# Kernel optimization log

Hardware: AMD Instinct MI355X
Metric: run time of the kernel (lower is better)

## Reference

```python
import jax, jax.numpy as jnp
import numpy as np

N = 50000      # n_nodes == ninput
E = 800000     # edges
NHID = 96
N_INTER = 6
EPS = 1e-12


def _l2norm(x):
    # F.normalize(x, p=2, dim=1) with eps=1e-12
    n = jnp.linalg.norm(x, axis=1, keepdims=True)
    return x / jnp.maximum(n, EPS)


def _sage(x, src, dst, Wl, bl, Wr, n):
    # PyG SAGEConv (mean aggr): lin_l(mean_{j in N(i)} x_j) + lin_r(x_i)
    agg = jax.ops.segment_sum(x[src], dst, num_segments=n)          # [N, nhid]
    deg = jax.ops.segment_sum(jnp.ones((src.shape[0],), x.dtype), dst, num_segments=n)
    agg = agg / jnp.maximum(deg, 1.0)[:, None]
    return agg @ Wl + bl + x @ Wr


def _mlp(x, W1, b1, W2, b2, W3, b3):
    # GNN-Bet score MLP (eval mode, dropout p=0): nhid -> 2*nhid -> 2*nhid -> 1
    h = jax.nn.relu(x @ W1 + b1)
    h = jax.nn.relu(h @ W2 + b2)
    return h @ W3 + b3


def setup_inputs() -> dict:
    key = jax.random.key(0)
    ks = jax.random.split(key, 16)
    s = 0.05
    inp = {
        'edge_index1': jax.random.randint(ks[0], (2, E), 0, N, dtype=jnp.int32),
        'edge_vals1': jax.random.uniform(ks[1], (E,), dtype=jnp.float32),
        'edge_index2': jax.random.randint(ks[2], (2, E), 0, N, dtype=jnp.int32),
        # GNN_Layer_Init: weight [ninput=N, nhid], bias [nhid]
        'gc1_W': jax.random.normal(ks[3], (N, NHID), dtype=jnp.float32) * s,
        'gc1_b': jnp.zeros((NHID,), jnp.float32),
        # 7 SAGEConv layers (6 intermediate + gc_last), stacked
        'sage_Wl': jax.random.normal(ks[4], (7, NHID, NHID), dtype=jnp.float32) * s,
        'sage_bl': jnp.zeros((7, NHID), jnp.float32),
        'sage_Wr': jax.random.normal(ks[5], (7, NHID, NHID), dtype=jnp.float32) * s,
        # score MLP
        'mlp_W1': jax.random.normal(ks[6], (NHID, 2 * NHID), dtype=jnp.float32) * s,
        'mlp_b1': jnp.zeros((2 * NHID,), jnp.float32),
        'mlp_W2': jax.random.normal(ks[7], (2 * NHID, 2 * NHID), dtype=jnp.float32) * s,
        'mlp_b2': jnp.zeros((2 * NHID,), jnp.float32),
        'mlp_W3': jax.random.normal(ks[8], (2 * NHID, 1), dtype=jnp.float32) * s,
        'mlp_b3': jnp.zeros((1,), jnp.float32),
    }
    return inp


def reference(edge_index1, edge_vals1, edge_index2, gc1_W, gc1_b,
              sage_Wl, sage_bl, sage_Wr,
              mlp_W1, mlp_b1, mlp_W2, mlp_b2, mlp_W3, mlp_b3):
    # gc1: spmm(adj1, W) -> out[i] = sum_j adj1[i,j] * W[j]
    dst1, src1 = edge_index1[0], edge_index1[1]
    h0 = jax.ops.segment_sum(gc1_W[src1] * edge_vals1[:, None], dst1, num_segments=N) + gc1_b
    x2_1 = _l2norm(jax.nn.relu(h0))

    src2, dst2 = edge_index2[0], edge_index2[1]

    # main trunk: 6 intermediate SAGE layers applied sequentially
    x = x2_1
    for i in range(N_INTER):
        x = _l2norm(jax.nn.relu(_sage(x, src2, dst2, sage_Wl[i], sage_bl[i], sage_Wr[i], N)))
    x_last = jax.nn.relu(_sage(x, src2, dst2, sage_Wl[N_INTER], sage_bl[N_INTER], sage_Wr[N_INTER], N))

    # scores: MLP on x2_1, on each intermediate layer applied once to x2_1, and on x_last
    score = _mlp(x2_1, mlp_W1, mlp_b1, mlp_W2, mlp_b2, mlp_W3, mlp_b3)
    for i in range(N_INTER):
        xi = _l2norm(jax.nn.relu(_sage(x2_1, src2, dst2, sage_Wl[i], sage_bl[i], sage_Wr[i], N)))
        score = score + _mlp(xi, mlp_W1, mlp_b1, mlp_W2, mlp_b2, mlp_W3, mlp_b3)
    score = score + _mlp(x_last, mlp_W1, mlp_b1, mlp_W2, mlp_b2, mlp_W3, mlp_b3)
    return score  # [N, 1]
```

## Files before the change

kernel.cpp:

```cpp
#include <hip/hip_runtime.h>

#define NH 96
#define NH2 192

typedef __attribute__((ext_vector_type(8))) short short8;
typedef __attribute__((ext_vector_type(4))) float f32x4;

__device__ __forceinline__ unsigned short f2b(float f) {
  unsigned u = __float_as_uint(f);
  unsigned r = (u + 0x7FFFu + ((u >> 16) & 1u)) >> 16;
  return (unsigned short)r;
}
__device__ __forceinline__ float blo(unsigned w) { return __uint_as_float(w << 16); }
__device__ __forceinline__ float bhi(unsigned w) { return __uint_as_float(w & 0xFFFF0000u); }
__device__ __forceinline__ float b2f(short v) { return __uint_as_float(((unsigned)(unsigned short)v) << 16); }

__device__ __forceinline__ unsigned cvt_pk(float lo, float hi) {
  unsigned r;
  asm("v_cvt_pk_bf16_f32 %0, %1, %2" : "=v"(r) : "v"(lo), "v"(hi));
  return r;
}

__device__ __forceinline__ short8 u4_to_s8(int a, int b, int c, int d) {
  union { int u[4]; short8 s; } x;
  x.u[0] = a; x.u[1] = b; x.u[2] = c; x.u[3] = d;
  return x.s;
}

#define MFMA(a, b, c) __builtin_amdgcn_mfma_f32_16x16x32_bf16((a), (b), (c), 0, 0, 0)
#define WFRAG(p, idx) (*(const short8*)((p) + ((idx) << 9) + (l << 3)))

__device__ __forceinline__ void stage(unsigned short* dst, const unsigned short* src, int nshorts,
                                      int tid, int nt) {
  const uint4* s = (const uint4*)src;
  uint4* d = (uint4*)dst;
  int nv = nshorts >> 3;
  for (int i = tid; i < nv; i += nt) d[i] = s[i];
}

__device__ __forceinline__ short8 xchg(unsigned p0lo, unsigned p0hi, unsigned p1lo, unsigned p1hi,
                                       int srcA, int srcB, int hi) {
  int a0 = __shfl((int)p0lo, srcA), a1 = __shfl((int)p0hi, srcA);
  int c0 = __shfl((int)p1lo, srcA), c1 = __shfl((int)p1hi, srcA);
  int b0 = __shfl((int)p0lo, srcB), b1 = __shfl((int)p0hi, srcB);
  int d0 = __shfl((int)p1lo, srcB), d1 = __shfl((int)p1hi, srcB);
  return u4_to_s8(hi ? c0 : a0, hi ? c1 : a1, hi ? d0 : b0, hi ? d1 : b1);
}

__device__ __forceinline__ void gather_mean(const int* __restrict__ rp, const int* __restrict__ csrc,
                                            const unsigned short* __restrict__ X,
                                            int nd, int g, short8 af[3]) {
  int s = rp[nd], e = rp[nd + 1];
  float aa[3][8], bb[3][8];
#pragma unroll
  for (int kf = 0; kf < 3; ++kf)
#pragma unroll
    for (int j = 0; j < 8; ++j) { aa[kf][j] = 0.f; bb[kf][j] = 0.f; }

  const unsigned short* Xg = X + g * 8;
  int i = s;
  for (; i + 3 < e; i += 4) {
    const unsigned short* x0 = Xg + (size_t)csrc[i] * NH;
    const unsigned short* x1 = Xg + (size_t)csrc[i + 1] * NH;
    const unsigned short* x2 = Xg + (size_t)csrc[i + 2] * NH;
    const unsigned short* x3 = Xg + (size_t)csrc[i + 3] * NH;
    short8 r00 = *(const short8*)(x0), r01 = *(const short8*)(x0 + 32), r02 = *(const short8*)(x0 + 64);
    short8 r10 = *(const short8*)(x1), r11 = *(const short8*)(x1 + 32), r12 = *(const short8*)(x1 + 64);
    short8 r20 = *(const short8*)(x2), r21 = *(const short8*)(x2 + 32), r22 = *(const short8*)(x2 + 64);
    short8 r30 = *(const short8*)(x3), r31 = *(const short8*)(x3 + 32), r32 = *(const short8*)(x3 + 64);
#pragma unroll
    for (int j = 0; j < 8; ++j) {
      aa[0][j] += b2f(r00[j]) + b2f(r20[j]);
      aa[1][j] += b2f(r01[j]) + b2f(r21[j]);
      aa[2][j] += b2f(r02[j]) + b2f(r22[j]);
      bb[0][j] += b2f(r10[j]) + b2f(r30[j]);
      bb[1][j] += b2f(r11[j]) + b2f(r31[j]);
      bb[2][j] += b2f(r12[j]) + b2f(r32[j]);
    }
  }
  for (; i < e; ++i) {
    const unsigned short* x0 = Xg + (size_t)csrc[i] * NH;
    short8 r0 = *(const short8*)(x0), r1 = *(const short8*)(x0 + 32), r2 = *(const short8*)(x0 + 64);
#pragma unroll
    for (int j = 0; j < 8; ++j) {
      aa[0][j] += b2f(r0[j]); aa[1][j] += b2f(r1[j]); aa[2][j] += b2f(r2[j]);
    }
  }
  float inv = 1.f / fmaxf((float)(e - s), 1.f);
#pragma unroll
  for (int kf = 0; kf < 3; ++kf)
#pragma unroll
    for (int j = 0; j < 8; ++j) af[kf][j] = (short)f2b((aa[kf][j] + bb[kf][j]) * inv);
}


__global__ void k_count(const int* __restrict__ dst1, const int* __restrict__ dst2,
                        int* __restrict__ cnt1, int* __restrict__ cnt2, int E, int psize, int cblocks,
                        const float* __restrict__ Wl, const float* __restrict__ Wr,
                        const float* __restrict__ W1, const float* __restrict__ W2,
                        const float* __restrict__ gW,
                        unsigned short* __restrict__ Wlp, unsigned short* __restrict__ Wrp,
                        unsigned short* __restrict__ W1p, unsigned short* __restrict__ W2p,
                        unsigned short* __restrict__ gwb, int gtotal) {
  if (blockIdx.x < (unsigned)cblocks) {
    int p = blockIdx.x & 7;
    int e = (blockIdx.x >> 3) * blockDim.x + threadIdx.x;
    if (e >= E) return;
    int lo = p * psize, hi = lo + psize;
    int d = dst1[e];
    if (d >= lo && d < hi) atomicAdd(&cnt1[d], 1);
    int dd = dst2[e];
    if (dd >= lo && dd < hi) atomicAdd(&cnt2[dd], 1);
    return;
  }
  int t = (blockIdx.x - cblocks) * blockDim.x + threadIdx.x;
  if (t < 129024) {
    bool isR = t >= 64512;
    int u = isR ? t - 64512 : t;
    int i = u / 9216, v = u % 9216;
    int tt = v / 1536, r = v % 1536;
    int kf = r / 512, w = r % 512, l = w >> 3, j = w & 7;
    int c = l & 15, g = l >> 4;
    int k = kf * 32 + g * 8 + j, nn = tt * 16 + c;
    float val = (isR ? Wr : Wl)[i * 9216 + k * 96 + nn];
    (isR ? Wrp : Wlp)[u] = f2b(val);
  } else if (t < 147456) {
    int u = t - 129024;
    int tt = u / 1536, r = u % 1536;
    int kf = r / 512, w = r % 512, l = w >> 3, j = w & 7;
    int c = l & 15, g = l >> 4;
    int k = kf * 32 + g * 8 + j, nn = tt * 16 + c;
    W1p[u] = f2b(W1[k * 192 + nn]);
  } else if (t < 184320) {
    int u = t - 147456;
    int tt = u / 3072, r = u % 3072;
    int kf = r / 512, w = r % 512, l = w >> 3, j = w & 7;
    int c = l & 15, g = l >> 4;
    int k = kf * 32 + g * 8 + j, nn = tt * 16 + c;
    W2p[u] = f2b(W2[k * 192 + nn]);
  } else {
    int i = (t - 184320) * 4;
    if (i + 3 < gtotal) {
      float4 v = *(const float4*)(gW + i);
      ushort4 o;
      o.x = f2b(v.x); o.y = f2b(v.y); o.z = f2b(v.z); o.w = f2b(v.w);
      *(ushort4*)(gwb + i) = o;
    }
  }
}


__global__ __launch_bounds__(256) void k_scanA(const int* __restrict__ cnt1, const int* __restrict__ cnt2,
                                               int* __restrict__ bs, int n) {
  int seg = blockIdx.y;
  const int* cnt = seg ? cnt2 : cnt1;
  int t = threadIdx.x;
  int idx = blockIdx.x * 1024 + t * 4;
  int sum = 0;
  if (idx + 3 < n) {
    int4 v = *(const int4*)(cnt + idx);
    sum = v.x + v.y + v.z + v.w;
  } else {
    for (int j = 0; j < 4; ++j) if (idx + j < n) sum += cnt[idx + j];
  }
  __shared__ int s[256];
  s[t] = sum;
  __syncthreads();
  for (int off = 128; off > 0; off >>= 1) {
    if (t < off) s[t] += s[t + off];
    __syncthreads();
  }
  if (t == 0) bs[seg * 64 + blockIdx.x] = s[0];
}

__global__ __launch_bounds__(128) void k_scanB(int* __restrict__ bs, int* __restrict__ rp1,
                                               int* __restrict__ rp2, int nb, int n) {
  int w = threadIdx.x >> 6, l = threadIdx.x & 63;
  int v = (l < nb) ? bs[w * 64 + l] : 0;
  int incl = v;
  for (int off = 1; off < 64; off <<= 1) {
    int u = __shfl_up(incl, off);
    if (l >= off) incl += u;
  }
  if (l < nb) bs[w * 64 + l] = incl - v;
  if (l == 63) {
    int* rp = w ? rp2 : rp1;
    rp[n] = incl;
  }
}

__global__ __launch_bounds__(256) void k_scanC(const int* __restrict__ cnt1, const int* __restrict__ cnt2,
                                               const int* __restrict__ bs,
                                               int* __restrict__ rp1, int* __restrict__ cur1,
                                               int* __restrict__ rp2, int* __restrict__ cur2, int n) {
  int seg = blockIdx.y;
  const int* cnt = seg ? cnt2 : cnt1;
  int* rp = seg ? rp2 : rp1;
  int* cur = seg ? cur2 : cur1;
  int t = threadIdx.x;
  int idx = blockIdx.x * 1024 + t * 4;
  int v[4] = {0, 0, 0, 0};
  if (idx + 3 < n) {
    int4 q = *(const int4*)(cnt + idx);
    v[0] = q.x; v[1] = q.y; v[2] = q.z; v[3] = q.w;
  } else {
    for (int j = 0; j < 4; ++j) if (idx + j < n) v[j] = cnt[idx + j];
  }
  int tsum = v[0] + v[1] + v[2] + v[3];
  __shared__ int s[256];
  s[t] = tsum;
  __syncthreads();
  for (int off = 1; off < 256; off <<= 1) {
    int u = (t >= off) ? s[t - off] : 0;
    __syncthreads();
    s[t] += u;
    __syncthreads();
  }
  int run = (t == 0 ? 0 : s[t - 1]) + bs[seg * 64 + blockIdx.x];
  for (int j = 0; j < 4; ++j) {
    if (idx + j < n) {
      rp[idx + j] = run;
      cur[idx + j] = run;
      run += v[j];
    }
  }
}

__global__ __launch_bounds__(1024) void k_scan(const int* __restrict__ cnt, int* __restrict__ rp,
                                               int* __restrict__ cur, int n) {
  __shared__ int s[1024];
  int tid = threadIdx.x;
  int chunk = (n + 1023) >> 10;
  int beg = tid * chunk;
  int end = min(beg + chunk, n);
  int sum = 0;
  for (int i = beg; i < end; ++i) sum += cnt[i];
  s[tid] = sum;
  __syncthreads();
  for (int off = 1; off < 1024; off <<= 1) {
    int v = (tid >= off) ? s[tid - off] : 0;
    __syncthreads();
    s[tid] += v;
    __syncthreads();
  }
  int excl = (tid == 0) ? 0 : s[tid - 1];
  for (int i = beg; i < end; ++i) { rp[i] = excl; cur[i] = excl; excl += cnt[i]; }
  if (tid == 1023) rp[n] = s[1023];
}

__global__ void k_scatter(const int* __restrict__ d1, const int* __restrict__ s1, const float* __restrict__ v1,
                          int* __restrict__ cur1, int2* __restrict__ c1sv,
                          const int* __restrict__ s2, const int* __restrict__ d2,
                          int* __restrict__ cur2, int* __restrict__ c2s, int E, int psize) {
  int p = blockIdx.x & 7;
  int e = (blockIdx.x >> 3) * blockDim.x + threadIdx.x;
  if (e >= E) return;
  int lo = p * psize, hi = lo + psize;
  int d = d1[e];
  if (d >= lo && d < hi) {
    int pos = atomicAdd(&cur1[d], 1);
    c1sv[pos] = make_int2(s1[e], __float_as_int(v1[e]));
  }
  int dd = d2[e];
  if (dd >= lo && dd < hi) {
    int pos = atomicAdd(&cur2[dd], 1);
    c2s[pos] = s2[e];
  }
}


__global__ __launch_bounds__(256) void k_gc1(const int* __restrict__ rp, const int2* __restrict__ cv,
                                             const unsigned short* __restrict__ Wb,
                                             const float* __restrict__ b, unsigned short* __restrict__ out, int n) {
  int gw = (blockIdx.x * 256 + threadIdx.x) >> 6;
  int l = threadIdx.x & 63;
  if (gw >= n) return;
  int s = rp[gw], e = rp[gw + 1];
  bool act = l < 48;
  float a0 = 0.f, a1 = 0.f, b0 = 0.f, b1 = 0.f, c0 = 0.f, c1 = 0.f, d0 = 0.f, d1 = 0.f;
  int i = s;
  for (; i + 3 < e; i += 4) {
    int2 q0 = cv[i], q1 = cv[i + 1], q2 = cv[i + 2], q3 = cv[i + 3];
    if (act) {
      unsigned w0 = *(const unsigned*)(Wb + (size_t)q0.x * NH + 2 * l);
      unsigned w1 = *(const unsigned*)(Wb + (size_t)q1.x * NH + 2 * l);
      unsigned w2 = *(const unsigned*)(Wb + (size_t)q2.x * NH + 2 * l);
      unsigned w3 = *(const unsigned*)(Wb + (size_t)q3.x * NH + 2 * l);
      float v0 = __int_as_float(q0.y), v1 = __int_as_float(q1.y);
      float v2 = __int_as_float(q2.y), v3 = __int_as_float(q3.y);
      a0 = fmaf(v0, blo(w0), a0); a1 = fmaf(v0, bhi(w0), a1);
      b0 = fmaf(v1, blo(w1), b0); b1 = fmaf(v1, bhi(w1), b1);
      c0 = fmaf(v2, blo(w2), c0); c1 = fmaf(v2, bhi(w2), c1);
      d0 = fmaf(v3, blo(w3), d0); d1 = fmaf(v3, bhi(w3), d1);
    }
  }
  for (; i < e; ++i) {
    int2 q0 = cv[i];
    if (act) {
      unsigned w0 = *(const unsigned*)(Wb + (size_t)q0.x * NH + 2 * l);
      float v0 = __int_as_float(q0.y);
      a0 = fmaf(v0, blo(w0), a0); a1 = fmaf(v0, bhi(w0), a1);
    }
  }
  a0 += b0 + c0 + d0; a1 += b1 + c1 + d1;
  if (act) {
    a0 = fmaxf(a0 + b[2 * l], 0.f);
    a1 = fmaxf(a1 + b[2 * l + 1], 0.f);
  } else { a0 = a1 = 0.f; }
  float ss = a0 * a0 + a1 * a1;
#pragma unroll
  for (int o = 1; o < 64; o <<= 1) ss += __shfl_xor(ss, o);
  float sc = 1.f / fmaxf(sqrtf(ss), 1e-12f);
  if (act) {
    unsigned pk = ((unsigned)f2b(a1 * sc) << 16) | f2b(a0 * sc);
    ((unsigned*)out)[(size_t)gw * 48 + l] = pk;
  }
}


__global__ __launch_bounds__(256) void k_agg(const int* __restrict__ rp, const int* __restrict__ csrc,
                                             const unsigned short* __restrict__ X,
                                             unsigned short* __restrict__ out, int n) {
  int gw = (blockIdx.x * 256 + threadIdx.x) >> 6;
  int l = threadIdx.x & 63;
  if (gw >= n) return;
  int s = rp[gw], e = rp[gw + 1];
  bool act = l < 48;
  float a0 = 0.f, a1 = 0.f, b0 = 0.f, b1 = 0.f, c0 = 0.f, c1 = 0.f, d0 = 0.f, d1 = 0.f;
  int i = s;
  for (; i + 3 < e; i += 4) {
    int s0 = csrc[i], s1 = csrc[i + 1], s2 = csrc[i + 2], s3 = csrc[i + 3];
    if (act) {
      unsigned w0 = *(const unsigned*)(X + (size_t)s0 * NH + 2 * l);
      unsigned w1 = *(const unsigned*)(X + (size_t)s1 * NH + 2 * l);
      unsigned w2 = *(const unsigned*)(X + (size_t)s2 * NH + 2 * l);
      unsigned w3 = *(const unsigned*)(X + (size_t)s3 * NH + 2 * l);
      a0 += blo(w0); a1 += bhi(w0);
      b0 += blo(w1); b1 += bhi(w1);
      c0 += blo(w2); c1 += bhi(w2);
      d0 += blo(w3); d1 += bhi(w3);
    }
  }
  for (; i < e; ++i) {
    int s0 = csrc[i];
    if (act) {
      unsigned w0 = *(const unsigned*)(X + (size_t)s0 * NH + 2 * l);
      a0 += blo(w0); a1 += bhi(w0);
    }
  }
  a0 += b0 + c0 + d0; a1 += b1 + c1 + d1;
  float inv = 1.f / fmaxf((float)(e - s), 1.f);
  if (act) {
    unsigned pk = ((unsigned)f2b(a1 * inv) << 16) | f2b(a0 * inv);
    ((unsigned*)out)[(size_t)gw * 48 + l] = pk;
  }
}


template <int EPI>
__device__ __forceinline__ void sage_body(int blk, int nwaves, unsigned short* sw,
                                          const int* __restrict__ rp, const int* __restrict__ csrc,
                                          const unsigned short* __restrict__ X,
                                          const unsigned short* __restrict__ Wlp,
                                          const unsigned short* __restrict__ Wrp,
                                          const float* __restrict__ bias,
                                          unsigned short* __restrict__ Y, int n) {
  int tid = threadIdx.x;
  int l = tid & 63;
  int m0 = (blk * nwaves + (tid >> 6)) * 16;
  int c = l & 15, g = l >> 4;

  stage(sw, Wlp, 9216, tid, nwaves * 64);
  stage(sw + 9216, Wrp, 9216, tid, nwaves * 64);
  __syncthreads();

  int nd = min(m0 + c, n - 1);
  short8 af[3];
  gather_mean(rp, csrc, X, nd, g, af);

  size_t aoff = (size_t)nd * NH + g * 8;
  short8 xf[3];
#pragma unroll
  for (int kf = 0; kf < 3; ++kf) xf[kf] = *(const short8*)(X + aoff + kf * 32);

  f32x4 acc[6];
#pragma unroll
  for (int t = 0; t < 6; ++t) acc[t] = (f32x4){0.f, 0.f, 0.f, 0.f};
#pragma unroll
  for (int kf = 0; kf < 3; ++kf) {
#pragma unroll
    for (int t = 0; t < 6; ++t) {
      short8 wlf = WFRAG(sw, t * 3 + kf);
      acc[t] = MFMA(wlf, af[kf], acc[t]);
    }
#pragma unroll
    for (int t = 0; t < 6; ++t) {
      short8 wrf = WFRAG(sw + 9216, t * 3 + kf);
      acc[t] = MFMA(wrf, xf[kf], acc[t]);
    }
  }

  float v[6][4];
  float ss = 0.f;
#pragma unroll
  for (int t = 0; t < 6; ++t) {
    float4 bv = *(const float4*)(bias + t * 16 + g * 4);
#pragma unroll
    for (int r = 0; r < 4; ++r) {
      float x = fmaxf(acc[t][r] + ((const float*)&bv)[r], 0.f);
      v[t][r] = x;
      ss = fmaf(x, x, ss);
    }
  }
  if (EPI == 0) {
    ss += __shfl_xor(ss, 16);
    ss += __shfl_xor(ss, 32);
    float sc = 1.f / fmaxf(sqrtf(ss), 1e-12f);
#pragma unroll
    for (int t = 0; t < 6; ++t)
#pragma unroll
      for (int r = 0; r < 4; ++r) v[t][r] *= sc;
  }
  if (m0 + c < n) {
    unsigned short* yr = Y + (size_t)(m0 + c) * NH;
#pragma unroll
    for (int t = 0; t < 6; ++t)
      *(uint2*)(yr + t * 16 + g * 4) = make_uint2(cvt_pk(v[t][0], v[t][1]), cvt_pk(v[t][2], v[t][3]));
  }
}

template <int EPI>
__global__ __launch_bounds__(256) void k_sageagg(const int* __restrict__ rp, const int* __restrict__ csrc,
                                                 const unsigned short* __restrict__ X,
                                                 const unsigned short* __restrict__ Wlp,
                                                 const unsigned short* __restrict__ Wrp,
                                                 const float* __restrict__ bias,
                                                 unsigned short* __restrict__ Y, int n) {
  __shared__ __align__(16) unsigned short sw[18432];
  sage_body<EPI>(blockIdx.x, 4, sw, rp, csrc, X, Wlp, Wrp, bias, Y, n);
}


__global__ __launch_bounds__(512) void k_last(const int* __restrict__ rp, const int* __restrict__ csrc,
                                              const unsigned short* __restrict__ X,
                                              const unsigned short* __restrict__ Wlp,
                                              const unsigned short* __restrict__ Wrp,
                                              const float* __restrict__ bias,
                                              const unsigned short* __restrict__ W1p, const float* __restrict__ b1,
                                              const unsigned short* __restrict__ W2p, const float* __restrict__ b2,
                                              const float* __restrict__ W3, const float* __restrict__ b3,
                                              float* __restrict__ score, int n) {
  __shared__ __align__(16) unsigned short sw[18432];
  int tid = threadIdx.x;
  int l = tid & 63;
  int m0 = (blockIdx.x * 8 + (tid >> 6)) * 16;
  int c = l & 15, g = l >> 4;
  int srcA = c + ((g & 1) << 5), srcB = srcA + 16, hi = g >> 1;

  stage(sw, Wlp, 9216, tid, 512);
  stage(sw + 9216, Wrp, 9216, tid, 512);
  __syncthreads();

  int nd = min(m0 + c, n - 1);
  short8 af[3];
  gather_mean(rp, csrc, X, nd, g, af);

  size_t aoff = (size_t)nd * NH + g * 8;
  short8 xf[3];
#pragma unroll
  for (int kf = 0; kf < 3; ++kf) xf[kf] = *(const short8*)(X + aoff + kf * 32);

  f32x4 acc[6];
#pragma unroll
  for (int t = 0; t < 6; ++t) acc[t] = (f32x4){0.f, 0.f, 0.f, 0.f};
#pragma unroll
  for (int kf = 0; kf < 3; ++kf) {
#pragma unroll
    for (int t = 0; t < 6; ++t) {
      short8 wlf = WFRAG(sw, t * 3 + kf);
      acc[t] = MFMA(wlf, af[kf], acc[t]);
    }
#pragma unroll
    for (int t = 0; t < 6; ++t) {
      short8 wrf = WFRAG(sw + 9216, t * 3 + kf);
      acc[t] = MFMA(wrf, xf[kf], acc[t]);
    }
  }

  unsigned pk[6][2];
#pragma unroll
  for (int t = 0; t < 6; ++t) {
    float4 bv = *(const float4*)(bias + t * 16 + g * 4);
    float x0 = fmaxf(acc[t][0] + bv.x, 0.f);
    float x1 = fmaxf(acc[t][1] + bv.y, 0.f);
    float x2 = fmaxf(acc[t][2] + bv.z, 0.f);
    float x3 = fmaxf(acc[t][3] + bv.w, 0.f);
    pk[t][0] = cvt_pk(x0, x1);
    pk[t][1] = cvt_pk(x2, x3);
  }

  __syncthreads();
  stage(sw, W1p, 18432, tid, 512);
  short8 af1[3];
#pragma unroll
  for (int kf = 0; kf < 3; ++kf)
    af1[kf] = xchg(pk[2 * kf][0], pk[2 * kf][1], pk[2 * kf + 1][0], pk[2 * kf + 1][1], srcA, srcB, hi);
  __syncthreads();

  unsigned pk1[12][2];
#pragma unroll
  for (int t = 0; t < 12; ++t) {
    f32x4 a0 = (f32x4){0.f, 0.f, 0.f, 0.f};
#pragma unroll
    for (int kf = 0; kf < 3; ++kf) {
      short8 wf = WFRAG(sw, t * 3 + kf);
      a0 = MFMA(wf, af1[kf], a0);
    }
    float4 bv = *(const float4*)(b1 + t * 16 + g * 4);
    pk1[t][0] = cvt_pk(fmaxf(a0[0] + bv.x, 0.f), fmaxf(a0[1] + bv.y, 0.f));
    pk1[t][1] = cvt_pk(fmaxf(a0[2] + bv.z, 0.f), fmaxf(a0[3] + bv.w, 0.f));
  }

  short8 af2[6];
#pragma unroll
  for (int kf = 0; kf < 6; ++kf)
    af2[kf] = xchg(pk1[2 * kf][0], pk1[2 * kf][1], pk1[2 * kf + 1][0], pk1[2 * kf + 1][1], srcA, srcB, hi);

  float sv = 0.f;
#pragma unroll
  for (int h = 0; h < 2; ++h) {
    __syncthreads();
    stage(sw, W2p + h * 18432, 18432, tid, 512);
    __syncthreads();
#pragma unroll
    for (int tt = 0; tt < 6; ++tt) {
      int t = h * 6 + tt;
      f32x4 a0 = (f32x4){0.f, 0.f, 0.f, 0.f};
#pragma unroll
      for (int kf = 0; kf < 6; ++kf) {
        short8 wf = WFRAG(sw, tt * 6 + kf);
        a0 = MFMA(wf, af2[kf], a0);
      }
      float4 bv = *(const float4*)(b2 + t * 16 + g * 4);
      float4 wv3 = *(const float4*)(W3 + t * 16 + g * 4);
#pragma unroll
      for (int r = 0; r < 4; ++r)
        sv = fmaf(fmaxf(a0[r] + ((const float*)&bv)[r], 0.f), ((const float*)&wv3)[r], sv);
    }
  }
  sv += __shfl_xor(sv, 16);
  sv += __shfl_xor(sv, 32);
  if (g == 0 && m0 + c < n) score[m0 + c] += sv + b3[0];
}


__device__ __forceinline__ void branch_body(int bb, int blk, unsigned short* sw,
                                            const unsigned short* __restrict__ Ag,
                                            const unsigned short* __restrict__ X21,
                                            const unsigned short* __restrict__ Wlp,
                                            const unsigned short* __restrict__ Wrp,
                                            const float* __restrict__ sbl,
                                            const unsigned short* __restrict__ W1p, const float* __restrict__ b1,
                                            const unsigned short* __restrict__ W2p, const float* __restrict__ b2,
                                            const float* __restrict__ W3, const float* __restrict__ b3,
                                            unsigned short* __restrict__ Xb, float* __restrict__ score, int n) {
  int tid = threadIdx.x;
  int l = tid & 63;
  int m0 = (blk * 8 + (tid >> 6)) * 32;
  int c = l & 15, g = l >> 4;
  int srcA = c + ((g & 1) << 5), srcB = srcA + 16, hi = g >> 1;
  int rA = min(m0 + c, n - 1), rB = min(m0 + 16 + c, n - 1);
  size_t aoffA = (size_t)rA * NH + g * 8, aoffB = (size_t)rB * NH + g * 8;

  short8 af1[2][3];

  if (bb < 6) {
    const float* bl = sbl + (size_t)bb * NH;
    stage(sw, Wlp + (size_t)bb * 9216, 9216, tid, 512);
    stage(sw + 9216, Wrp + (size_t)bb * 9216, 9216, tid, 512);

    short8 agf[2][3], xf[2][3];
#pragma unroll
    for (int kf = 0; kf < 3; ++kf) {
      agf[0][kf] = *(const short8*)(Ag + aoffA + kf * 32);
      agf[1][kf] = *(const short8*)(Ag + aoffB + kf * 32);
      xf[0][kf] = *(const short8*)(X21 + aoffA + kf * 32);
      xf[1][kf] = *(const short8*)(X21 + aoffB + kf * 32);
    }
    __syncthreads();

    float v[2][6][4];
    float ss0 = 0.f, ss1 = 0.f;
#pragma unroll
    for (int t = 0; t < 6; ++t) {
      f32x4 a0 = (f32x4){0.f, 0.f, 0.f, 0.f};
      f32x4 a1 = (f32x4){0.f, 0.f, 0.f, 0.f};
#pragma unroll
      for (int kf = 0; kf < 3; ++kf) {
        short8 wlf = WFRAG(sw, t * 3 + kf);
        a0 = MFMA(wlf, agf[0][kf], a0);
        a1 = MFMA(wlf, agf[1][kf], a1);
        short8 wrf = WFRAG(sw + 9216, t * 3 + kf);
        a0 = MFMA(wrf, xf[0][kf], a0);
        a1 = MFMA(wrf, xf[1][kf], a1);
      }
      float4 bv = *(const float4*)(bl + t * 16 + g * 4);
#pragma unroll
      for (int r = 0; r < 4; ++r) {
        float x0 = fmaxf(a0[r] + ((const float*)&bv)[r], 0.f);
        float x1 = fmaxf(a1[r] + ((const float*)&bv)[r], 0.f);
        v[0][t][r] = x0; ss0 = fmaf(x0, x0, ss0);
        v[1][t][r] = x1; ss1 = fmaf(x1, x1, ss1);
      }
    }
    ss0 += __shfl_xor(ss0, 16); ss0 += __shfl_xor(ss0, 32);
    ss1 += __shfl_xor(ss1, 16); ss1 += __shfl_xor(ss1, 32);
    float sc0 = 1.f / fmaxf(sqrtf(ss0), 1e-12f);
    float sc1 = 1.f / fmaxf(sqrtf(ss1), 1e-12f);

    unsigned pk[2][6][2];
#pragma unroll
    for (int t = 0; t < 6; ++t) {
      pk[0][t][0] = cvt_pk(v[0][t][0] * sc0, v[0][t][1] * sc0);
      pk[0][t][1] = cvt_pk(v[0][t][2] * sc0, v[0][t][3] * sc0);
      pk[1][t][0] = cvt_pk(v[1][t][0] * sc1, v[1][t][1] * sc1);
      pk[1][t][1] = cvt_pk(v[1][t][2] * sc1, v[1][t][3] * sc1);
    }
    if (bb == 0) {
      if (m0 + c < n) {
        unsigned short* yr = Xb + (size_t)(m0 + c) * NH;
#pragma unroll
        for (int t = 0; t < 6; ++t) *(uint2*)(yr + t * 16 + g * 4) = make_uint2(pk[0][t][0], pk[0][t][1]);
      }
      if (m0 + 16 + c < n) {
        unsigned short* yr = Xb + (size_t)(m0 + 16 + c) * NH;
#pragma unroll
        for (int t = 0; t < 6; ++t) *(uint2*)(yr + t * 16 + g * 4) = make_uint2(pk[1][t][0], pk[1][t][1]);
      }
    }

    __syncthreads();
    stage(sw, W1p, 18432, tid, 512);
#pragma unroll
    for (int kf = 0; kf < 3; ++kf) {
      af1[0][kf] = xchg(pk[0][2 * kf][0], pk[0][2 * kf][1], pk[0][2 * kf + 1][0], pk[0][2 * kf + 1][1], srcA, srcB, hi);
      af1[1][kf] = xchg(pk[1][2 * kf][0], pk[1][2 * kf][1], pk[1][2 * kf + 1][0], pk[1][2 * kf + 1][1], srcA, srcB, hi);
    }
    __syncthreads();
  } else {
#pragma unroll
    for (int kf = 0; kf < 3; ++kf) {
      af1[0][kf] = *(const short8*)(X21 + aoffA + kf * 32);
      af1[1][kf] = *(const short8*)(X21 + aoffB + kf * 32);
    }
    stage(sw, W1p, 18432, tid, 512);
    __syncthreads();
  }

  unsigned pk1[2][12][2];
#pragma unroll
  for (int t = 0; t < 12; ++t) {
    f32x4 a0 = (f32x4){0.f, 0.f, 0.f, 0.f};
    f32x4 a1 = (f32x4){0.f, 0.f, 0.f, 0.f};
#pragma unroll
    for (int kf = 0; kf < 3; ++kf) {
      short8 wf = WFRAG(sw, t * 3 + kf);
      a0 = MFMA(wf, af1[0][kf], a0);
      a1 = MFMA(wf, af1[1][kf], a1);
    }
    float4 bv = *(const float4*)(b1 + t * 16 + g * 4);
    pk1[0][t][0] = cvt_pk(fmaxf(a0[0] + bv.x, 0.f), fmaxf(a0[1] + bv.y, 0.f));
    pk1[0][t][1] = cvt_pk(fmaxf(a0[2] + bv.z, 0.f), fmaxf(a0[3] + bv.w, 0.f));
    pk1[1][t][0] = cvt_pk(fmaxf(a1[0] + bv.x, 0.f), fmaxf(a1[1] + bv.y, 0.f));
    pk1[1][t][1] = cvt_pk(fmaxf(a1[2] + bv.z, 0.f), fmaxf(a1[3] + bv.w, 0.f));
  }

  short8 af2[2][6];
#pragma unroll
  for (int kf = 0; kf < 6; ++kf) {
    af2[0][kf] = xchg(pk1[0][2 * kf][0], pk1[0][2 * kf][1], pk1[0][2 * kf + 1][0], pk1[0][2 * kf + 1][1], srcA, srcB, hi);
    af2[1][kf] = xchg(pk1[1][2 * kf][0], pk1[1][2 * kf][1], pk1[1][2 * kf + 1][0], pk1[1][2 * kf + 1][1], srcA, srcB, hi);
  }
  float sv0 = 0.f, sv1 = 0.f;
#pragma unroll
  for (int h = 0; h < 2; ++h) {
    __syncthreads();
    stage(sw, W2p + h * 18432, 18432, tid, 512);
    __syncthreads();
#pragma unroll
    for (int tt = 0; tt < 6; ++tt) {
      int t = h * 6 + tt;
      f32x4 a0 = (f32x4){0.f, 0.f, 0.f, 0.f};
      f32x4 a1 = (f32x4){0.f, 0.f, 0.f, 0.f};
#pragma unroll
      for (int kf = 0; kf < 6; ++kf) {
        short8 wf = WFRAG(sw, tt * 6 + kf);
        a0 = MFMA(wf, af2[0][kf], a0);
        a1 = MFMA(wf, af2[1][kf], a1);
      }
      float4 bv = *(const float4*)(b2 + t * 16 + g * 4);
      float4 wv3 = *(const float4*)(W3 + t * 16 + g * 4);
#pragma unroll
      for (int r = 0; r < 4; ++r) {
        sv0 = fmaf(fmaxf(a0[r] + ((const float*)&bv)[r], 0.f), ((const float*)&wv3)[r], sv0);
        sv1 = fmaf(fmaxf(a1[r] + ((const float*)&bv)[r], 0.f), ((const float*)&wv3)[r], sv1);
      }
    }
  }
  sv0 += __shfl_xor(sv0, 16); sv0 += __shfl_xor(sv0, 32);
  sv1 += __shfl_xor(sv1, 16); sv1 += __shfl_xor(sv1, 32);
  if (g == 0) {
    float b3v = b3[0];
    if (m0 + c < n) atomicAdd(&score[m0 + c], sv0 + b3v);
    if (m0 + 16 + c < n) atomicAdd(&score[m0 + 16 + c], sv1 + b3v);
  }
}

__global__ __launch_bounds__(512) void k_branchA(const unsigned short* __restrict__ Ag,
                                                 const unsigned short* __restrict__ X21,
                                                 const unsigned short* __restrict__ Wlp,
                                                 const unsigned short* __restrict__ Wrp,
                                                 const float* __restrict__ sbl,
                                                 const unsigned short* __restrict__ W1p, const float* __restrict__ b1,
                                                 const unsigned short* __restrict__ W2p, const float* __restrict__ b2,
                                                 const float* __restrict__ W3, const float* __restrict__ b3,
                                                 unsigned short* __restrict__ Xb, float* __restrict__ score,
                                                 int n, int nblk) {
  __shared__ __align__(16) unsigned short sw[18432];
  int bb = (blockIdx.x >= (unsigned)nblk) ? 6 : 0;
  int blk = blockIdx.x - (bb ? nblk : 0);
  branch_body(bb, blk, sw, Ag, X21, Wlp, Wrp, sbl, W1p, b1, W2p, b2, W3, b3, Xb, score, n);
}

__global__ __launch_bounds__(512) void k_mega(const unsigned short* __restrict__ Ag,
                                              const unsigned short* __restrict__ X21,
                                              const unsigned short* __restrict__ Wlp,
                                              const unsigned short* __restrict__ Wrp,
                                              const float* __restrict__ sbl,
                                              const unsigned short* __restrict__ W1p, const float* __restrict__ b1,
                                              const unsigned short* __restrict__ W2p, const float* __restrict__ b2,
                                              const float* __restrict__ W3, const float* __restrict__ b3,
                                              float* __restrict__ score,
                                              const int* __restrict__ rp2, const int* __restrict__ c2s,
                                              const unsigned short* __restrict__ Xb, unsigned short* __restrict__ Tb,
                                              int n, int nblk, int nbranch) {
  __shared__ __align__(16) unsigned short sw[18432];
  if (blockIdx.x < (unsigned)nbranch) {
    int bb = 1 + blockIdx.x / nblk;
    int blk = blockIdx.x - (bb - 1) * nblk;
    branch_body(bb, blk, sw, Ag, X21, Wlp, Wrp, sbl, W1p, b1, W2p, b2, W3, b3, nullptr, score, n);
  } else {
    sage_body<0>(blockIdx.x - nbranch, 8, sw, rp2, c2s, Xb,
                 Wlp + 9216, Wrp + 9216, sbl + NH, Tb, n);
  }
}


extern "C" void kernel_launch(void* const* d_in, const int* in_sizes, int n_in,
                              void* d_out, int out_size, void* d_ws, size_t ws_size,
                              hipStream_t stream) {
  const int* ei1 = (const int*)d_in[0];
  const float* ev1 = (const float*)d_in[1];
  const int* ei2 = (const int*)d_in[2];
  const float* gW = (const float*)d_in[3];
  const float* gb = (const float*)d_in[4];
  const float* sWl = (const float*)d_in[5];
  const float* sbl = (const float*)d_in[6];
  const float* sWr = (const float*)d_in[7];
  const float* W1 = (const float*)d_in[8];
  const float* b1 = (const float*)d_in[9];
  const float* W2 = (const float*)d_in[10];
  const float* b2 = (const float*)d_in[11];
  const float* W3 = (const float*)d_in[12];
  const float* b3 = (const float*)d_in[13];
  float* score = (float*)d_out;

  const int E = in_sizes[0] / 2;
  const int n = in_sizes[3] / NH;

  const int* d1 = ei1;
  const int* s1 = ei1 + E;
  const int* s2 = ei2;
  const int* d2 = ei2 + E;

  char* w = (char*)d_ws;
  auto alloc = [&](size_t bytes) {
    char* p = w;
    w += (bytes + 255) & ~(size_t)255;
    return p;
  };
  int* cnt1 = (int*)alloc((size_t)n * 4);
  int* cnt2 = (int*)alloc((size_t)n * 4);
  int* cur1 = (int*)alloc((size_t)n * 4);
  int* cur2 = (int*)alloc((size_t)n * 4);
  int* rp1 = (int*)alloc((size_t)(n + 1) * 4);
  int* rp2 = (int*)alloc((size_t)(n + 1) * 4);
  int* bs = (int*)alloc(128 * 4);
  int2* c1sv = (int2*)alloc((size_t)E * 8);
  int* c2s = (int*)alloc((size_t)E * 4);
  unsigned short* gwb = (unsigned short*)alloc((size_t)n * NH * 2);
  unsigned short* wlp = (unsigned short*)alloc((size_t)7 * NH * NH * 2);
  unsigned short* wrp = (unsigned short*)alloc((size_t)7 * NH * NH * 2);
  unsigned short* w1p = (unsigned short*)alloc((size_t)NH * NH2 * 2);
  unsigned short* w2p = (unsigned short*)alloc((size_t)NH2 * NH2 * 2);
  unsigned short* x21 = (unsigned short*)alloc((size_t)n * NH * 2);
  unsigned short* Ag = (unsigned short*)alloc((size_t)n * NH * 2);
  unsigned short* xb = (unsigned short*)alloc((size_t)n * NH * 2);
  unsigned short* tb = (unsigned short*)alloc((size_t)n * NH * 2);

  size_t zbytes = (size_t)((char*)cur1 - (char*)cnt1) + (size_t)n * 4;
  hipMemsetAsync(cnt1, 0, zbytes, stream);
  hipMemsetAsync(score, 0, (size_t)n * 4, stream);

  int eb = (E + 255) / 256;
  int nb4 = (n + 3) / 4;
  int sblk = (n + 63) / 64;
  int nblk = (n + 255) / 256;
  int tblk8 = (n + 127) / 128;
  int psize = (n + 7) / 8;
  int nb1024 = (n + 1023) / 1024;
  int gtotal = n * NH;
  int prep_blocks = (184320 + gtotal / 4 + 255) / 256;

  k_count<<<eb * 8 + prep_blocks, 256, 0, stream>>>(d1, d2, cnt1, cnt2, E, psize, eb * 8,
                                                    sWl, sWr, W1, W2, gW, wlp, wrp, w1p, w2p, gwb, gtotal);
  if (nb1024 <= 64) {
    k_scanA<<<dim3(nb1024, 2), 256, 0, stream>>>(cnt1, cnt2, bs, n);
    k_scanB<<<1, 128, 0, stream>>>(bs, rp1, rp2, nb1024, n);
    k_scanC<<<dim3(nb1024, 2), 256, 0, stream>>>(cnt1, cnt2, bs, rp1, cur1, rp2, cur2, n);
  } else {
    k_scan<<<1, 1024, 0, stream>>>(cnt1, rp1, cur1, n);
    k_scan<<<1, 1024, 0, stream>>>(cnt2, rp2, cur2, n);
  }
  k_scatter<<<eb * 8, 256, 0, stream>>>(d1, s1, ev1, cur1, c1sv, s2, d2, cur2, c2s, E, psize);

  k_gc1<<<nb4, 256, 0, stream>>>(rp1, c1sv, gwb, gb, x21, n);

  k_agg<<<nb4, 256, 0, stream>>>(rp2, c2s, x21, Ag, n);

  k_branchA<<<2 * nblk, 512, 0, stream>>>(Ag, x21, wlp, wrp, sbl, w1p, b1, w2p, b2, W3, b3,
                                          xb, score, n, nblk);

  k_mega<<<5 * nblk + tblk8, 512, 0, stream>>>(Ag, x21, wlp, wrp, sbl, w1p, b1, w2p, b2, W3, b3,
                                               score, rp2, c2s, xb, tb, n, nblk, 5 * nblk);

  unsigned short* xc = tb;
  unsigned short* xn = xb;
  for (int i = 2; i < 6; ++i) {
    k_sageagg<0><<<sblk, 256, 0, stream>>>(rp2, c2s, xc, wlp + (size_t)i * 9216,
                                           wrp + (size_t)i * 9216, sbl + (size_t)i * NH, xn, n);
    unsigned short* tmp = xc; xc = xn; xn = tmp;
  }

  k_last<<<tblk8, 512, 0, stream>>>(rp2, c2s, xc, wlp + (size_t)6 * 9216, wrp + (size_t)6 * 9216,
                                    sbl + (size_t)6 * NH, w1p, b1, w2p, b2, W3, b3, score, n);

  (void)n_in; (void)out_size; (void)ws_size;
}
```

Baseline: 557.7 us.

## Sort nodes by in-degree so SAGE waves process similar-degree rows together

Builds a degree histogram, scans it, and writes a permutation that buckets nodes by in-degree in the second graph. The SAGE aggregation kernels (the intermediate layers, the mega kernel's trunk layer and the last layer) index nodes through this permutation and write outputs and scores at the permuted node. Each 16-node MFMA tile then holds nodes with similar neighbour counts, which is meant to cut idle lanes in the gather loop. In exchange it adds three small launches plus an extra indirection, and it scatters row writes and self-row reads, which loses contiguous memory locality.

Result: slower. 830.9 us (+49.0%).

```diff
diff --git a/kernel.cpp b/kernel.cpp
--- a/kernel.cpp
+++ b/kernel.cpp
@@ -248,6 +248,37 @@
   if (tid == 1023) rp[n] = s[1023];
 }
 
+
+__global__ void k_hist(const int* __restrict__ rp, int* __restrict__ hist, int n) {
+  int t = blockIdx.x * blockDim.x + threadIdx.x;
+  if (t < n) atomicAdd(&hist[min(rp[t + 1] - rp[t], 511)], 1);
+}
+
+__global__ __launch_bounds__(512) void k_hscan(const int* __restrict__ hist, int* __restrict__ hcur) {
+  __shared__ int s[512];
+  int t = threadIdx.x;
+  int v = hist[t];
+  s[t] = v;
+  __syncthreads();
+  for (int off = 1; off < 512; off <<= 1) {
+    int u = (t >= off) ? s[t - off] : 0;
+    __syncthreads();
+    s[t] += u;
+    __syncthreads();
+  }
+  hcur[t] = s[t] - v;
+}
+
+__global__ void k_perm(const int* __restrict__ rp, int* __restrict__ hcur,
+                       int* __restrict__ perm, int n) {
+  int t = blockIdx.x * blockDim.x + threadIdx.x;
+  if (t < n) {
+    int b = min(rp[t + 1] - rp[t], 511);
+    int slot = atomicAdd(&hcur[b], 1);
+    perm[slot] = t;
+  }
+}
+
 __global__ void k_scatter(const int* __restrict__ d1, const int* __restrict__ s1, const float* __restrict__ v1,
                           int* __restrict__ cur1, int2* __restrict__ c1sv,
                           const int* __restrict__ s2, const int* __restrict__ d2,
@@ -360,6 +391,7 @@
 template <int EPI>
 __device__ __forceinline__ void sage_body(int blk, int nwaves, unsigned short* sw,
                                           const int* __restrict__ rp, const int* __restrict__ csrc,
+                                          const int* __restrict__ perm,
                                           const unsigned short* __restrict__ X,
                                           const unsigned short* __restrict__ Wlp,
                                           const unsigned short* __restrict__ Wrp,
@@ -374,7 +406,7 @@
   stage(sw + 9216, Wrp, 9216, tid, nwaves * 64);
   __syncthreads();
 
-  int nd = min(m0 + c, n - 1);
+  int nd = perm[min(m0 + c, n - 1)];
   short8 af[3];
   gather_mean(rp, csrc, X, nd, g, af);
 
@@ -422,7 +454,7 @@
       for (int r = 0; r < 4; ++r) v[t][r] *= sc;
   }
   if (m0 + c < n) {
-    unsigned short* yr = Y + (size_t)(m0 + c) * NH;
+    unsigned short* yr = Y + (size_t)nd * NH;
 #pragma unroll
     for (int t = 0; t < 6; ++t)
       *(uint2*)(yr + t * 16 + g * 4) = make_uint2(cvt_pk(v[t][0], v[t][1]), cvt_pk(v[t][2], v[t][3]));
@@ -431,17 +463,19 @@
 
 template <int EPI>
 __global__ __launch_bounds__(256) void k_sageagg(const int* __restrict__ rp, const int* __restrict__ csrc,
+                                                 const int* __restrict__ perm,
                                                  const unsigned short* __restrict__ X,
                                                  const unsigned short* __restrict__ Wlp,
                                                  const unsigned short* __restrict__ Wrp,
                                                  const float* __restrict__ bias,
                                                  unsigned short* __restrict__ Y, int n) {
   __shared__ __align__(16) unsigned short sw[18432];
-  sage_body<EPI>(blockIdx.x, 4, sw, rp, csrc, X, Wlp, Wrp, bias, Y, n);
+  sage_body<EPI>(blockIdx.x, 4, sw, rp, csrc, perm, X, Wlp, Wrp, bias, Y, n);
 }
 
 
 __global__ __launch_bounds__(512) void k_last(const int* __restrict__ rp, const int* __restrict__ csrc,
+                                              const int* __restrict__ perm,
                                               const unsigned short* __restrict__ X,
                                               const unsigned short* __restrict__ Wlp,
                                               const unsigned short* __restrict__ Wrp,
@@ -461,7 +495,7 @@
   stage(sw + 9216, Wrp, 9216, tid, 512);
   __syncthreads();
 
-  int nd = min(m0 + c, n - 1);
+  int nd = perm[min(m0 + c, n - 1)];
   short8 af[3];
   gather_mean(rp, csrc, X, nd, g, af);
 
@@ -550,7 +584,7 @@
   }
   sv += __shfl_xor(sv, 16);
   sv += __shfl_xor(sv, 32);
-  if (g == 0 && m0 + c < n) score[m0 + c] += sv + b3[0];
+  if (g == 0 && m0 + c < n) score[nd] += sv + b3[0];
 }
 
 
@@ -742,6 +776,7 @@
                                               const float* __restrict__ W3, const float* __restrict__ b3,
                                               float* __restrict__ score,
                                               const int* __restrict__ rp2, const int* __restrict__ c2s,
+                                              const int* __restrict__ perm,
                                               const unsigned short* __restrict__ Xb, unsigned short* __restrict__ Tb,
                                               int n, int nblk, int nbranch) {
   __shared__ __align__(16) unsigned short sw[18432];
@@ -750,7 +785,7 @@
     int blk = blockIdx.x - (bb - 1) * nblk;
     branch_body(bb, blk, sw, Ag, X21, Wlp, Wrp, sbl, W1p, b1, W2p, b2, W3, b3, nullptr, score, n);
   } else {
-    sage_body<0>(blockIdx.x - nbranch, 8, sw, rp2, c2s, Xb,
+    sage_body<0>(blockIdx.x - nbranch, 8, sw, rp2, c2s, perm, Xb,
                  Wlp + 9216, Wrp + 9216, sbl + NH, Tb, n);
   }
 }
@@ -791,8 +826,11 @@
   };
   int* cnt1 = (int*)alloc((size_t)n * 4);
   int* cnt2 = (int*)alloc((size_t)n * 4);
+  int* hist = (int*)alloc(512 * 4);
   int* cur1 = (int*)alloc((size_t)n * 4);
   int* cur2 = (int*)alloc((size_t)n * 4);
+  int* hcur = (int*)alloc(512 * 4);
+  int* perm = (int*)alloc((size_t)n * 4);
   int* rp1 = (int*)alloc((size_t)(n + 1) * 4);
   int* rp2 = (int*)alloc((size_t)(n + 1) * 4);
   int* bs = (int*)alloc(128 * 4);
@@ -808,7 +846,7 @@
   unsigned short* xb = (unsigned short*)alloc((size_t)n * NH * 2);
   unsigned short* tb = (unsigned short*)alloc((size_t)n * NH * 2);
 
-  size_t zbytes = (size_t)((char*)cur1 - (char*)cnt1) + (size_t)n * 4;
+  size_t zbytes = (size_t)((char*)cur1 - (char*)cnt1);
   hipMemsetAsync(cnt1, 0, zbytes, stream);
   hipMemsetAsync(score, 0, (size_t)n * 4, stream);
 
@@ -821,6 +859,7 @@
   int nb1024 = (n + 1023) / 1024;
   int gtotal = n * NH;
   int prep_blocks = (184320 + gtotal / 4 + 255) / 256;
+  int nb256 = (n + 255) / 256;
 
   k_count<<<eb * 8 + prep_blocks, 256, 0, stream>>>(d1, d2, cnt1, cnt2, E, psize, eb * 8,
                                                     sWl, sWr, W1, W2, gW, wlp, wrp, w1p, w2p, gwb, gtotal);
@@ -834,6 +873,10 @@
   }
   k_scatter<<<eb * 8, 256, 0, stream>>>(d1, s1, ev1, cur1, c1sv, s2, d2, cur2, c2s, E, psize);
 
+  k_hist<<<nb256, 256, 0, stream>>>(rp2, hist, n);
+  k_hscan<<<1, 512, 0, stream>>>(hist, hcur);
+  k_perm<<<nb256, 256, 0, stream>>>(rp2, hcur, perm, n);
+
   k_gc1<<<nb4, 256, 0, stream>>>(rp1, c1sv, gwb, gb, x21, n);
 
   k_agg<<<nb4, 256, 0, stream>>>(rp2, c2s, x21, Ag, n);
@@ -842,17 +885,17 @@
                                           xb, score, n, nblk);
 
   k_mega<<<5 * nblk + tblk8, 512, 0, stream>>>(Ag, x21, wlp, wrp, sbl, w1p, b1, w2p, b2, W3, b3,
-                                               score, rp2, c2s, xb, tb, n, nblk, 5 * nblk);
+                                               score, rp2, c2s, perm, xb, tb, n, 5 * nblk / 5, 5 * nblk);
 
   unsigned short* xc = tb;
   unsigned short* xn = xb;
   for (int i = 2; i < 6; ++i) {
-    k_sageagg<0><<<sblk, 256, 0, stream>>>(rp2, c2s, xc, wlp + (size_t)i * 9216,
+    k_sageagg<0><<<sblk, 256, 0, stream>>>(rp2, c2s, perm, xc, wlp + (size_t)i * 9216,
                                            wrp + (size_t)i * 9216, sbl + (size_t)i * NH, xn, n);
     unsigned short* tmp = xc; xc = xn; xn = tmp;
   }
 
-  k_last<<<tblk8, 512, 0, stream>>>(rp2, c2s, xc, wlp + (size_t)6 * 9216, wrp + (size_t)6 * 9216,
+  k_last<<<tblk8, 512, 0, stream>>>(rp2, c2s, perm, xc, wlp + (size_t)6 * 9216, wrp + (size_t)6 * 9216,
                                     sbl + (size_t)6 * NH, w1p, b1, w2p, b2, W3, b3, score, n);
 
   (void)n_in; (void)out_size; (void)ws_size;
```
